# Optimization experiments

Hardware: AMD Instinct MI355X
Metric: run time of the kernel (lower is better)

Reference implementation:

```python
import jax, jax.numpy as jnp
import numpy as np

B, N, D = 4, 2048, 512
H, C = 8, 64  # heads, dim_head; inner_dim = H*C = 512
SCALE = C ** -0.5


def setup_inputs() -> dict:
    key = jax.random.key(0)
    ks = jax.random.split(key, 6)
    s = 0.02
    return {
        "x": jax.random.normal(ks[0], (B, N, D), jnp.float32),
        "Wq": jax.random.normal(ks[1], (D, H * C), jnp.float32) * s,
        "Wk": jax.random.normal(ks[2], (D, H * C), jnp.float32) * s,
        "Wv": jax.random.normal(ks[3], (D, H * C), jnp.float32) * s,
        "Wo": jax.random.normal(ks[4], (H * C, D), jnp.float32) * s,
        "bo": jnp.zeros((D,), jnp.float32),
    }


def reference(x, Wq, Wk, Wv, Wo, bo):
    # projections (bias-free, as in the torch module)
    q = (x @ Wq).reshape(B, N, H, C)
    k = (x @ Wk).reshape(B, N, H, C)
    v = (x @ Wv).reshape(B, N, H, C)
    # scores: [B, H, N, N]
    sim = jnp.einsum("bihc,bjhc->bhij", q, k) * SCALE
    attn = jax.nn.softmax(sim, axis=-1)
    out = jnp.einsum("bhij,bjhc->bihc", attn, v).reshape(B, N, H * C)
    # output projection (Dropout(0.0) is identity)
    return out @ Wo + bo
```

## Files before the change

kernel.cpp:

```cpp
#include <hip/hip_runtime.h>

using bf16x8 = __attribute__((ext_vector_type(8))) short;
using f32x4  = __attribute__((ext_vector_type(4))) float;
typedef unsigned short u16;

#if __has_builtin(__builtin_amdgcn_exp2f)
#define EXP2F __builtin_amdgcn_exp2f
#else
#define EXP2F exp2f
#endif

__device__ __forceinline__ u16 f2bf(float f) {
    unsigned int u = __float_as_uint(f);
    u += 0x7FFFu + ((u >> 16) & 1u);
    return (u16)(u >> 16);
}

__device__ __forceinline__ unsigned int cvtpk_bf16(float a, float b) {
    unsigned int r;
    asm("v_cvt_pk_bf16_f32 %0, %1, %2" : "=v"(r) : "v"(a), "v"(b));
    return r;
}

__device__ __forceinline__ void gload16(const void* g, void* l) {
    __builtin_amdgcn_global_load_lds(
        (const __attribute__((address_space(1))) void*)g,
        (__attribute__((address_space(3))) void*)l, 16, 0, 0);
}

__global__ __launch_bounds__(256) void k_convert_x(const float* __restrict__ x,
                                                   u16* __restrict__ xb, int n8) {
    int i = blockIdx.x * 256 + threadIdx.x;
    if (i >= n8) return;
    const float4* p = (const float4*)(x + (size_t)i * 8);
    float4 a = p[0], b = p[1];
    bf16x8 v;
    v[0] = (short)f2bf(a.x); v[1] = (short)f2bf(a.y);
    v[2] = (short)f2bf(a.z); v[3] = (short)f2bf(a.w);
    v[4] = (short)f2bf(b.x); v[5] = (short)f2bf(b.y);
    v[6] = (short)f2bf(b.z); v[7] = (short)f2bf(b.w);
    *(bf16x8*)(xb + (size_t)i * 8) = v;
}

__global__ __launch_bounds__(256) void k_transpose_all(
    const float* __restrict__ W0, const float* __restrict__ W1,
    const float* __restrict__ W2, const float* __restrict__ W3,
    u16* __restrict__ Wt) {
    __shared__ float tile[32][33];
    const float* W = (blockIdx.z == 0) ? W0 : (blockIdx.z == 1) ? W1
                   : (blockIdx.z == 2) ? W2 : W3;
    u16* dst = Wt + (size_t)blockIdx.z * 262144;
    int jb = blockIdx.x * 32, kb = blockIdx.y * 32;
    int tx = threadIdx.x, ty = threadIdx.y;
    #pragma unroll
    for (int i = 0; i < 32; i += 8)
        tile[ty + i][tx] = W[(size_t)(kb + ty + i) * 512 + jb + tx];
    __syncthreads();
    #pragma unroll
    for (int i = 0; i < 32; i += 8)
        dst[(size_t)(jb + ty + i) * 512 + kb + tx] = f2bf(tile[tx][ty + i]);
}

__global__ __launch_bounds__(256) void k_gemm_qkv(
    const u16* __restrict__ xb, const u16* __restrict__ wt,
    u16* __restrict__ q_ws, u16* __restrict__ k_ws, u16* __restrict__ v_ws)
{
    __shared__ __align__(16) u16 A_lds[128 * 32];
    __shared__ __align__(16) u16 B_lds[128 * 32];
    const int t = threadIdx.x;
    const int lane = t & 63, w = t >> 6;
    const int lr = lane & 15, lg = lane >> 4;
    const int wm = w >> 1, wn = w & 1;
    const int mb = blockIdx.y * 128, nb = blockIdx.x * 128;
    const char* abytes = (const char*)xb;
    const char* bbytes = (const char*)(wt + (size_t)blockIdx.z * 262144);
    const int srow = (w << 4) + (lane >> 2);
    const int scol = (lane & 3) << 4;

    f32x4 acc[4][4];
    #pragma unroll
    for (int i = 0; i < 4; ++i)
        #pragma unroll
        for (int j = 0; j < 4; ++j) acc[i][j] = (f32x4){0.f, 0.f, 0.f, 0.f};

    for (int kt = 0; kt < 512; kt += 32) {
        gload16(abytes + ((size_t)(mb + srow) * 512 + kt) * 2 + scol,
                (char*)A_lds + (w << 10));
        gload16(abytes + ((size_t)(mb + srow + 64) * 512 + kt) * 2 + scol,
                (char*)A_lds + 4096 + (w << 10));
        gload16(bbytes + ((size_t)(nb + srow) * 512 + kt) * 2 + scol,
                (char*)B_lds + (w << 10));
        gload16(bbytes + ((size_t)(nb + srow + 64) * 512 + kt) * 2 + scol,
                (char*)B_lds + 4096 + (w << 10));
        __syncthreads();
        bf16x8 af[4], bfr[4];
        #pragma unroll
        for (int f = 0; f < 4; ++f)
            af[f] = *(const bf16x8*)((const char*)A_lds + (size_t)(wm * 64 + f * 16 + lr) * 64 + (lg << 4));
        #pragma unroll
        for (int f = 0; f < 4; ++f)
            bfr[f] = *(const bf16x8*)((const char*)B_lds + (size_t)(wn * 64 + f * 16 + lr) * 64 + (lg << 4));
        #pragma unroll
        for (int fm = 0; fm < 4; ++fm)
            #pragma unroll
            for (int fc = 0; fc < 4; ++fc)
                acc[fm][fc] = __builtin_amdgcn_mfma_f32_16x16x32_bf16(af[fm], bfr[fc], acc[fm][fc], 0, 0, 0);
        __syncthreads();
    }

    const int z = blockIdx.z;
    u16* dst = (z == 0) ? q_ws : (z == 1) ? k_ws : v_ws;
    const float scale = (z == 0) ? 0.18033688011111827f : 1.0f;
    #pragma unroll
    for (int fm = 0; fm < 4; ++fm) {
        int row = mb + wm * 64 + fm * 16 + lg * 4;
        int bq = row >> 11, n = row & 2047;
        #pragma unroll
        for (int fc = 0; fc < 4; ++fc) {
            int col = nb + wn * 64 + fc * 16 + lr;
            int hh = col >> 6, c = col & 63;
            u16* p = dst + (((size_t)(bq * 8 + hh) * 2048) + n) * 64 + c;
            p[0]   = f2bf(acc[fm][fc][0] * scale);
            p[64]  = f2bf(acc[fm][fc][1] * scale);
            p[128] = f2bf(acc[fm][fc][2] * scale);
            p[192] = f2bf(acc[fm][fc][3] * scale);
        }
    }
}

__global__ __launch_bounds__(256) void k_transpose_v(const u16* __restrict__ v,
                                                     u16* __restrict__ vt) {
    __shared__ u16 tile[64][68];
    const int bh = blockIdx.y;
    const int n0 = blockIdx.x * 64;
    const u16* src = v + (size_t)bh * 2048 * 64;
    u16* dst = vt + (size_t)bh * 64 * 2048;
    const int t = threadIdx.x;
    const int nl = t >> 4, c4 = (t & 15) * 4;
    #pragma unroll
    for (int i = 0; i < 4; ++i)
        *(ushort4*)&tile[nl + 16 * i][c4] =
            *(const ushort4*)(src + (size_t)(n0 + nl + 16 * i) * 64 + c4);
    __syncthreads();
    const int n4 = (t & 15) * 4, cl = t >> 4;
    #pragma unroll
    for (int ci = 0; ci < 4; ++ci) {
        int c = cl + 16 * ci;
        ushort4 o;
        o.x = tile[n4][c]; o.y = tile[n4 + 1][c];
        o.z = tile[n4 + 2][c]; o.w = tile[n4 + 3][c];
        *(ushort4*)(dst + (size_t)c * 2048 + n0 + n4) = o;
    }
}

__global__ __launch_bounds__(512) void k_attn(
    const u16* __restrict__ q_ws, const u16* __restrict__ k_ws,
    const u16* __restrict__ vt_ws, u16* __restrict__ ao)
{
    __shared__ __align__(16) u16 Kb[2][4096];
    __shared__ __align__(16) u16 Vb[2][4096];
    __shared__ __align__(16) u16 Pl[128 * 64];

    const int t = threadIdx.x;
    const int lane = t & 63, w = t >> 6;
    const int lr = lane & 15, lg = lane >> 4;
    const int q0 = blockIdx.x * 128;
    const int bh = blockIdx.y, b = bh >> 3, h = bh & 7;

    const char* kbytes = (const char*)k_ws + (size_t)bh * (2048 * 128);
    const char* vbytes = (const char*)vt_ws + (size_t)bh * (64 * 4096);
    const char* qbytes = (const char*)q_ws + (size_t)bh * (2048 * 128);

    bf16x8 qf[2];
    #pragma unroll
    for (int kk = 0; kk < 2; ++kk)
        qf[kk] = *(const bf16x8*)(qbytes + (size_t)(q0 + w * 16 + lr) * 128 + kk * 64 + (lg << 4));

    const int srow = t >> 3;
    const int scb  = ((t & 7) << 4) ^ ((srow & 7) << 4);
    const int swzm = (lr & 7) << 4;

    float l_acc = 0.f;
    f32x4 acc_o[4];
    #pragma unroll
    for (int i = 0; i < 4; ++i) acc_o[i] = (f32x4){0.f, 0.f, 0.f, 0.f};

    auto stage = [&](int buf, int kv0) {
        gload16(kbytes + (size_t)(kv0 + srow) * 128 + scb,
                (char*)Kb + buf * 8192 + (w << 10));
        gload16(vbytes + (size_t)srow * 4096 + (size_t)kv0 * 2 + scb,
                (char*)Vb + buf * 8192 + (w << 10));
    };

    stage(0, 0);
    __syncthreads();
    int buf = 0;

    for (int tix = 0; tix < 32; ++tix) {
        if (tix < 31) stage(buf ^ 1, (tix + 1) * 64);

        const char* kbase = (const char*)Kb + buf * 8192;
        const char* vbase = (const char*)Vb + buf * 8192;

        f32x4 s[4];
        #pragma unroll
        for (int f = 0; f < 4; ++f) {
            const int rowb = (f * 16 + lr) * 128;
            bf16x8 ka0 = *(const bf16x8*)(kbase + rowb + ((lg << 4) ^ swzm));
            bf16x8 ka1 = *(const bf16x8*)(kbase + rowb + ((64 + (lg << 4)) ^ swzm));
            f32x4 a = (f32x4){0.f, 0.f, 0.f, 0.f};
            a = __builtin_amdgcn_mfma_f32_16x16x32_bf16(ka0, qf[0], a, 0, 0, 0);
            a = __builtin_amdgcn_mfma_f32_16x16x32_bf16(ka1, qf[1], a, 0, 0, 0);
            s[f] = a;
        }

        #pragma unroll
        for (int f = 0; f < 4; ++f) {
            float p0 = EXP2F(s[f][0]), p1 = EXP2F(s[f][1]);
            float p2 = EXP2F(s[f][2]), p3 = EXP2F(s[f][3]);
            l_acc += (p0 + p1) + (p2 + p3);
            uint2 pk;
            pk.x = cvtpk_bf16(p0, p1);
            pk.y = cvtpk_bf16(p2, p3);
            *(uint2*)((char*)Pl + (size_t)(w * 16 + lr) * 128 + (((f << 5) + (lg << 3)) ^ swzm)) = pk;
        }

        #pragma unroll
        for (int kk = 0; kk < 2; ++kk) {
            bf16x8 pa = *(const bf16x8*)((char*)Pl + (size_t)(w * 16 + lr) * 128 + (((kk << 6) + (lg << 4)) ^ swzm));
            #pragma unroll
            for (int fc = 0; fc < 4; ++fc) {
                bf16x8 vbF = *(const bf16x8*)(vbase + (size_t)(fc * 16 + lr) * 128 + (((kk << 6) + (lg << 4)) ^ swzm));
                acc_o[fc] = __builtin_amdgcn_mfma_f32_16x16x32_bf16(pa, vbF, acc_o[fc], 0, 0, 0);
            }
        }
        __syncthreads();
        buf ^= 1;
    }

    l_acc += __shfl_xor(l_acc, 16);
    l_acc += __shfl_xor(l_acc, 32);
    float linv = 1.0f / l_acc;
    float li0 = __shfl(linv, (lg << 2) + 0);
    float li1 = __shfl(linv, (lg << 2) + 1);
    float li2 = __shfl(linv, (lg << 2) + 2);
    float li3 = __shfl(linv, (lg << 2) + 3);
    u16* aobase = ao + ((size_t)b * 2048 + q0 + w * 16 + lg * 4) * 512 + h * 64;
    #pragma unroll
    for (int fc = 0; fc < 4; ++fc) {
        int c = fc * 16 + lr;
        aobase[c]        = f2bf(acc_o[fc][0] * li0);
        aobase[512 + c]  = f2bf(acc_o[fc][1] * li1);
        aobase[1024 + c] = f2bf(acc_o[fc][2] * li2);
        aobase[1536 + c] = f2bf(acc_o[fc][3] * li3);
    }
}

__global__ __launch_bounds__(256) void k_gemm_out(
    const u16* __restrict__ ain, const u16* __restrict__ wtO,
    const float* __restrict__ bo, float* __restrict__ out)
{
    __shared__ __align__(16) u16 A_lds[128 * 32];
    __shared__ __align__(16) u16 B_lds[128 * 32];
    const int t = threadIdx.x;
    const int lane = t & 63, w = t >> 6;
    const int lr = lane & 15, lg = lane >> 4;
    const int wm = w >> 1, wn = w & 1;
    const int mb = blockIdx.y * 128, nb = blockIdx.x * 128;
    const char* abytes = (const char*)ain;
    const char* bbytes = (const char*)wtO;
    const int srow = (w << 4) + (lane >> 2);
    const int scol = (lane & 3) << 4;

    f32x4 acc[4][4];
    #pragma unroll
    for (int i = 0; i < 4; ++i)
        #pragma unroll
        for (int j = 0; j < 4; ++j) acc[i][j] = (f32x4){0.f, 0.f, 0.f, 0.f};

    for (int kt = 0; kt < 512; kt += 32) {
        gload16(abytes + ((size_t)(mb + srow) * 512 + kt) * 2 + scol,
                (char*)A_lds + (w << 10));
        gload16(abytes + ((size_t)(mb + srow + 64) * 512 + kt) * 2 + scol,
                (char*)A_lds + 4096 + (w << 10));
        gload16(bbytes + ((size_t)(nb + srow) * 512 + kt) * 2 + scol,
                (char*)B_lds + (w << 10));
        gload16(bbytes + ((size_t)(nb + srow + 64) * 512 + kt) * 2 + scol,
                (char*)B_lds + 4096 + (w << 10));
        __syncthreads();
        bf16x8 af[4], bfr[4];
        #pragma unroll
        for (int f = 0; f < 4; ++f)
            af[f] = *(const bf16x8*)((const char*)A_lds + (size_t)(wm * 64 + f * 16 + lr) * 64 + (lg << 4));
        #pragma unroll
        for (int f = 0; f < 4; ++f)
            bfr[f] = *(const bf16x8*)((const char*)B_lds + (size_t)(wn * 64 + f * 16 + lr) * 64 + (lg << 4));
        #pragma unroll
        for (int fm = 0; fm < 4; ++fm)
            #pragma unroll
            for (int fc = 0; fc < 4; ++fc)
                acc[fm][fc] = __builtin_amdgcn_mfma_f32_16x16x32_bf16(af[fm], bfr[fc], acc[fm][fc], 0, 0, 0);
        __syncthreads();
    }

    float bias[4];
    #pragma unroll
    for (int fc = 0; fc < 4; ++fc) bias[fc] = bo[nb + wn * 64 + fc * 16 + lr];
    #pragma unroll
    for (int fm = 0; fm < 4; ++fm) {
        int row = mb + wm * 64 + fm * 16 + lg * 4;
        #pragma unroll
        for (int fc = 0; fc < 4; ++fc) {
            int col = nb + wn * 64 + fc * 16 + lr;
            float* p = out + (size_t)row * 512 + col;
            p[0]    = acc[fm][fc][0] + bias[fc];
            p[512]  = acc[fm][fc][1] + bias[fc];
            p[1024] = acc[fm][fc][2] + bias[fc];
            p[1536] = acc[fm][fc][3] + bias[fc];
        }
    }
}

extern "C" void kernel_launch(void* const* d_in, const int* in_sizes, int n_in,
                              void* d_out, int out_size, void* d_ws, size_t ws_size,
                              hipStream_t stream) {
    (void)in_sizes; (void)n_in; (void)out_size; (void)ws_size;
    const float* x  = (const float*)d_in[0];
    const float* Wq = (const float*)d_in[1];
    const float* Wk = (const float*)d_in[2];
    const float* Wv = (const float*)d_in[3];
    const float* Wo = (const float*)d_in[4];
    const float* bo = (const float*)d_in[5];
    float* out = (float*)d_out;

    char* ws = (char*)d_ws;
    u16* xb    = (u16*)(ws);
    u16* wt    = (u16*)(ws + 8388608);
    u16* q_ws  = (u16*)(ws + 10485760);
    u16* k_ws  = (u16*)(ws + 18874368);
    u16* v_ws  = (u16*)(ws + 27262976);
    u16* vt_ws = (u16*)(ws + 35651584);
    u16* ao    = v_ws;

    k_convert_x<<<2048, 256, 0, stream>>>(x, xb, 524288);
    k_transpose_all<<<dim3(16, 16, 4), dim3(32, 8), 0, stream>>>(Wq, Wk, Wv, Wo, wt);
    k_gemm_qkv<<<dim3(4, 64, 3), 256, 0, stream>>>(xb, wt, q_ws, k_ws, v_ws);
    k_transpose_v<<<dim3(32, 32), 256, 0, stream>>>(v_ws, vt_ws);
    k_attn<<<dim3(16, 32), 512, 0, stream>>>(q_ws, k_ws, vt_ws, ao);
    k_gemm_out<<<dim3(4, 64), 256, 0, stream>>>(ao, wt + 786432, bo, out);
}
```

Measured before the change: 165.9 us.

## Switch attention to 32x32x16 MFMA with register-resident P via permlane swap

The attention kernel moves from 16x16x32 to 32x32x16 bf16 MFMA tiles, with each of four waves owning 32 query rows instead of eight waves owning 16. The softmax probabilities are now kept in registers and rearranged into the PV operand layout with v_permlane32_swap, which removes the LDS round trip through the Pl buffer. Block size drops to 256 threads, so each wave issues two K/V async loads per stage. The trade-off is more accumulator registers per wave and fewer waves per block to hide latency.

```diff
diff --git a/kernel.cpp b/kernel.cpp
--- a/kernel.cpp
+++ b/kernel.cpp
@@ -2,7 +2,9 @@
 
 using bf16x8 = __attribute__((ext_vector_type(8))) short;
 using f32x4  = __attribute__((ext_vector_type(4))) float;
+using f32x16 = __attribute__((ext_vector_type(16))) float;
 typedef unsigned short u16;
+typedef unsigned int u32;
 
 #if __has_builtin(__builtin_amdgcn_exp2f)
 #define EXP2F __builtin_amdgcn_exp2f
@@ -16,10 +18,14 @@
     return (u16)(u >> 16);
 }
 
-__device__ __forceinline__ unsigned int cvtpk_bf16(float a, float b) {
-    unsigned int r;
+__device__ __forceinline__ u32 cvtpk_bf16(float a, float b) {
+    u32 r;
     asm("v_cvt_pk_bf16_f32 %0, %1, %2" : "=v"(r) : "v"(a), "v"(b));
     return r;
+}
+
+__device__ __forceinline__ void permswap32(u32& a, u32& b) {
+    asm volatile("v_permlane32_swap_b32 %0, %1" : "+v"(a), "+v"(b));
 }
 
 __device__ __forceinline__ void gload16(const void* g, void* l) {
@@ -153,17 +159,17 @@
     }
 }
 
-__global__ __launch_bounds__(512) void k_attn(
+__global__ __launch_bounds__(256) void k_attn(
     const u16* __restrict__ q_ws, const u16* __restrict__ k_ws,
     const u16* __restrict__ vt_ws, u16* __restrict__ ao)
 {
     __shared__ __align__(16) u16 Kb[2][4096];
     __shared__ __align__(16) u16 Vb[2][4096];
-    __shared__ __align__(16) u16 Pl[128 * 64];
 
     const int t = threadIdx.x;
     const int lane = t & 63, w = t >> 6;
-    const int lr = lane & 15, lg = lane >> 4;
+    const int hw = lane >> 5;
+    const int q32 = lane & 31;
     const int q0 = blockIdx.x * 128;
     const int bh = blockIdx.y, b = bh >> 3, h = bh & 7;
 
@@ -171,25 +177,28 @@
     const char* vbytes = (const char*)vt_ws + (size_t)bh * (64 * 4096);
     const char* qbytes = (const char*)q_ws + (size_t)bh * (2048 * 128);
 
-    bf16x8 qf[2];
-    #pragma unroll
-    for (int kk = 0; kk < 2; ++kk)
-        qf[kk] = *(const bf16x8*)(qbytes + (size_t)(q0 + w * 16 + lr) * 128 + kk * 64 + (lg << 4));
-
-    const int srow = t >> 3;
-    const int scb  = ((t & 7) << 4) ^ ((srow & 7) << 4);
-    const int swzm = (lr & 7) << 4;
+    bf16x8 qf[4];
+    #pragma unroll
+    for (int cs = 0; cs < 4; ++cs)
+        qf[cs] = *(const bf16x8*)(qbytes + (size_t)(q0 + w * 32 + q32) * 128 + cs * 32 + hw * 16);
+
+    const int sr8 = lane >> 3;
+    const int scw = ((lane & 7) << 4) ^ (sr8 << 4);
+    const int swz = (q32 & 7) << 4;
 
     float l_acc = 0.f;
-    f32x4 acc_o[4];
-    #pragma unroll
-    for (int i = 0; i < 4; ++i) acc_o[i] = (f32x4){0.f, 0.f, 0.f, 0.f};
+    f32x16 accA = (f32x16)(0.f), accB = (f32x16)(0.f);
 
     auto stage = [&](int buf, int kv0) {
-        gload16(kbytes + (size_t)(kv0 + srow) * 128 + scb,
-                (char*)Kb + buf * 8192 + (w << 10));
-        gload16(vbytes + (size_t)srow * 4096 + (size_t)kv0 * 2 + scb,
-                (char*)Vb + buf * 8192 + (w << 10));
+        #pragma unroll
+        for (int i = 0; i < 2; ++i) {
+            const int c = w * 2 + i;
+            const int row = c * 8 + sr8;
+            gload16(kbytes + (size_t)(kv0 + row) * 128 + scw,
+                    (char*)Kb + buf * 8192 + c * 1024 + (lane << 4));
+            gload16(vbytes + (size_t)row * 4096 + (size_t)kv0 * 2 + scw,
+                    (char*)Vb + buf * 8192 + c * 1024 + (lane << 4));
+        }
     };
 
     stage(0, 0);
@@ -202,57 +211,57 @@
         const char* kbase = (const char*)Kb + buf * 8192;
         const char* vbase = (const char*)Vb + buf * 8192;
 
-        f32x4 s[4];
-        #pragma unroll
-        for (int f = 0; f < 4; ++f) {
-            const int rowb = (f * 16 + lr) * 128;
-            bf16x8 ka0 = *(const bf16x8*)(kbase + rowb + ((lg << 4) ^ swzm));
-            bf16x8 ka1 = *(const bf16x8*)(kbase + rowb + ((64 + (lg << 4)) ^ swzm));
-            f32x4 a = (f32x4){0.f, 0.f, 0.f, 0.f};
-            a = __builtin_amdgcn_mfma_f32_16x16x32_bf16(ka0, qf[0], a, 0, 0, 0);
-            a = __builtin_amdgcn_mfma_f32_16x16x32_bf16(ka1, qf[1], a, 0, 0, 0);
-            s[f] = a;
-        }
-
-        #pragma unroll
-        for (int f = 0; f < 4; ++f) {
-            float p0 = EXP2F(s[f][0]), p1 = EXP2F(s[f][1]);
-            float p2 = EXP2F(s[f][2]), p3 = EXP2F(s[f][3]);
-            l_acc += (p0 + p1) + (p2 + p3);
-            uint2 pk;
-            pk.x = cvtpk_bf16(p0, p1);
-            pk.y = cvtpk_bf16(p2, p3);
-            *(uint2*)((char*)Pl + (size_t)(w * 16 + lr) * 128 + (((f << 5) + (lg << 3)) ^ swzm)) = pk;
-        }
-
-        #pragma unroll
-        for (int kk = 0; kk < 2; ++kk) {
-            bf16x8 pa = *(const bf16x8*)((char*)Pl + (size_t)(w * 16 + lr) * 128 + (((kk << 6) + (lg << 4)) ^ swzm));
-            #pragma unroll
-            for (int fc = 0; fc < 4; ++fc) {
-                bf16x8 vbF = *(const bf16x8*)(vbase + (size_t)(fc * 16 + lr) * 128 + (((kk << 6) + (lg << 4)) ^ swzm));
-                acc_o[fc] = __builtin_amdgcn_mfma_f32_16x16x32_bf16(pa, vbF, acc_o[fc], 0, 0, 0);
-            }
+        f32x16 s0 = (f32x16)(0.f), s1 = (f32x16)(0.f);
+        #pragma unroll
+        for (int cs = 0; cs < 4; ++cs) {
+            const int cbyte = (cs * 32 + hw * 16) ^ swz;
+            bf16x8 kf0 = *(const bf16x8*)(kbase + (size_t)q32 * 128 + cbyte);
+            bf16x8 kf1 = *(const bf16x8*)(kbase + (size_t)(32 + q32) * 128 + cbyte);
+            s0 = __builtin_amdgcn_mfma_f32_32x32x16_bf16(kf0, qf[cs], s0, 0, 0, 0);
+            s1 = __builtin_amdgcn_mfma_f32_32x32x16_bf16(kf1, qf[cs], s1, 0, 0, 0);
+        }
+
+        u32 pA[8], pB[8];
+        #pragma unroll
+        for (int m = 0; m < 8; ++m) {
+            float a0 = EXP2F(s0[2 * m]), a1 = EXP2F(s0[2 * m + 1]);
+            float b0 = EXP2F(s1[2 * m]), b1 = EXP2F(s1[2 * m + 1]);
+            l_acc += (a0 + a1) + (b0 + b1);
+            pA[m] = cvtpk_bf16(a0, a1);
+            pB[m] = cvtpk_bf16(b0, b1);
+        }
+
+        #pragma unroll
+        for (int ksg = 0; ksg < 4; ++ksg) {
+            const int ks = ksg & 1;
+            u32 a0 = (ksg < 2) ? pA[4 * ks]     : pB[4 * ks];
+            u32 a1 = (ksg < 2) ? pA[4 * ks + 1] : pB[4 * ks + 1];
+            u32 b0 = (ksg < 2) ? pA[4 * ks + 2] : pB[4 * ks + 2];
+            u32 b1 = (ksg < 2) ? pA[4 * ks + 3] : pB[4 * ks + 3];
+            permswap32(a0, b0);
+            permswap32(a1, b1);
+            union { u32 u[4]; bf16x8 v; } pf;
+            pf.u[0] = a0; pf.u[1] = a1; pf.u[2] = b0; pf.u[3] = b1;
+            const int kbyte = (ksg * 32 + hw * 16) ^ swz;
+            bf16x8 vf0 = *(const bf16x8*)(vbase + (size_t)q32 * 128 + kbyte);
+            bf16x8 vf1 = *(const bf16x8*)(vbase + (size_t)(32 + q32) * 128 + kbyte);
+            accA = __builtin_amdgcn_mfma_f32_32x32x16_bf16(pf.v, vf0, accA, 0, 0, 0);
+            accB = __builtin_amdgcn_mfma_f32_32x32x16_bf16(pf.v, vf1, accB, 0, 0, 0);
         }
         __syncthreads();
         buf ^= 1;
     }
 
-    l_acc += __shfl_xor(l_acc, 16);
     l_acc += __shfl_xor(l_acc, 32);
-    float linv = 1.0f / l_acc;
-    float li0 = __shfl(linv, (lg << 2) + 0);
-    float li1 = __shfl(linv, (lg << 2) + 1);
-    float li2 = __shfl(linv, (lg << 2) + 2);
-    float li3 = __shfl(linv, (lg << 2) + 3);
-    u16* aobase = ao + ((size_t)b * 2048 + q0 + w * 16 + lg * 4) * 512 + h * 64;
-    #pragma unroll
-    for (int fc = 0; fc < 4; ++fc) {
-        int c = fc * 16 + lr;
-        aobase[c]        = f2bf(acc_o[fc][0] * li0);
-        aobase[512 + c]  = f2bf(acc_o[fc][1] * li1);
-        aobase[1024 + c] = f2bf(acc_o[fc][2] * li2);
-        aobase[1536 + c] = f2bf(acc_o[fc][3] * li3);
+    const float linv = 1.0f / l_acc;
+
+    u16* aobase = ao + ((size_t)b * 2048 + q0 + w * 32) * 512 + h * 64;
+    #pragma unroll
+    for (int r = 0; r < 16; ++r) {
+        const int qrow = (r & 3) + 8 * (r >> 2) + 4 * hw;
+        const float li = __shfl(linv, qrow);
+        aobase[(size_t)qrow * 512 + q32]      = f2bf(accA[r] * li);
+        aobase[(size_t)qrow * 512 + 32 + q32] = f2bf(accB[r] * li);
     }
 }
 
@@ -346,6 +355,6 @@
     k_transpose_all<<<dim3(16, 16, 4), dim3(32, 8), 0, stream>>>(Wq, Wk, Wv, Wo, wt);
     k_gemm_qkv<<<dim3(4, 64, 3), 256, 0, stream>>>(xb, wt, q_ws, k_ws, v_ws);
     k_transpose_v<<<dim3(32, 32), 256, 0, stream>>>(v_ws, vt_ws);
-    k_attn<<<dim3(16, 32), 512, 0, stream>>>(q_ws, k_ws, vt_ws, ao);
+    k_attn<<<dim3(16, 32), 256, 0, stream>>>(q_ws, k_ws, vt_ws, ao);
     k_gemm_out<<<dim3(4, 64), 256, 0, stream>>>(ao, wt + 786432, bo, out);
 }
```

Result: slower. 171.6 us (+3.4%).
